# Performance work log

Measured on AMD Instinct MI355X. Metric: run time of the kernel, lower is better.

Reference implementation:

```python
import jax, jax.numpy as jnp
import numpy as np

MIN_NORM = 1e-15
PROJ_EPS = 4e-3   # HGCN PoincareBall eps for float32
C = 1.0
N_NODES = 100000
DEG = 5
F_IN = 128


def _artanh(x):
    return jnp.arctanh(jnp.clip(x, -1.0 + 1e-7, 1.0 - 1e-7))


def _norm(x):
    # clamped L2 norm over last dim, keepdims
    return jnp.maximum(jnp.sqrt(jnp.sum(x * x, axis=-1, keepdims=True)), MIN_NORM)


def proj(x, c):
    norm = _norm(x)
    maxnorm = (1.0 - PROJ_EPS) / jnp.sqrt(c)
    return jnp.where(norm > maxnorm, x / norm * maxnorm, x)


def expmap0(u, c):
    sc = jnp.sqrt(c)
    un = _norm(u)
    return jnp.tanh(sc * un) * u / (sc * un)


def logmap0(p, c):
    sc = jnp.sqrt(c)
    pn = _norm(p)
    return p / pn / sc * _artanh(sc * pn)


def mobius_matvec(m, x, c):
    # HGCN convention: mx = x @ m^T
    sc = jnp.sqrt(c)
    x_norm = _norm(x)
    mx = x @ m.T
    mx_norm = _norm(mx)
    res = jnp.tanh(mx_norm / x_norm * _artanh(sc * x_norm)) * mx / (mx_norm * sc)
    zero = jnp.all(mx == 0, axis=-1, keepdims=True)
    return jnp.where(zero, jnp.zeros_like(res), res)


def setup_inputs() -> dict:
    key = jax.random.key(0)
    k1, k2, k3, k4 = jax.random.split(key, 4)
    x = jax.random.normal(k1, (N_NODES, F_IN), jnp.float32) * 0.1
    gain = 1.414
    W = jax.random.normal(k2, (F_IN, F_IN), jnp.float32) * gain * np.sqrt(2.0 / (F_IN + F_IN))
    a = jax.random.normal(k3, (1, 2 * F_IN), jnp.float32) * gain * np.sqrt(2.0 / (1 + 2 * F_IN))
    # edge list: every node has DEG out-edges so row-sum normalization is safe
    src = jnp.repeat(jnp.arange(N_NODES, dtype=jnp.int32), DEG)
    dst = jax.random.randint(k4, (N_NODES * DEG,), 0, N_NODES, jnp.int32)
    edge = jnp.stack([src, dst])  # [2, E]
    return {"x": x, "edge": edge, "W": W, "a": a}


def reference(x, edge, W, a):
    c = C
    N = x.shape[0]
    # h = logmap0(proj(mobius_matvec(x, W)))  -> [F, N] (module's transposed layout)
    h = logmap0(proj(mobius_matvec(x, W, c), c), c)
    src, dst = edge[0], edge[1]
    # per-edge gather: [2F, E]
    edge_h = jnp.concatenate([h[:, src], h[:, dst]], axis=0)
    edge_h = proj(expmap0(edge_h, c), c)
    # mobius_matvec(edge_h.T, a) -> a @ edge_h : [1, E] -> [E]
    ee = jnp.squeeze(mobius_matvec(edge_h.T, a, c))
    ee = logmap0(proj(ee, c), c)
    ee = jnp.exp(-jax.nn.gelu(ee, approximate=False))  # positive edge weights
    # sparse spmm row-sum and aggregation (scatter-add by source node)
    e_rowsum = jax.ops.segment_sum(ee, src, num_segments=N)                     # [N]
    h_prime = jax.ops.segment_sum(ee[:, None] * h.T[dst], src, num_segments=N)  # [N, F]
    h_prime = h_prime / e_rowsum[:, None]
    return proj(expmap0(jax.nn.elu(h_prime), c), c)
```

## Files before the change

### kernel.cpp

```cpp
#include <hip/hip_runtime.h>
#include <math.h>

#define F 128
#define DEG 5
#define TM 128
#define MAXNORM_D 0.996
#define MIN_NORM_D 1e-15

typedef float f32x4 __attribute__((ext_vector_type(4)));
typedef short s16x8 __attribute__((ext_vector_type(8)));

__device__ inline double atanh_clip(double v) {
    v = fmin(fmax(v, -1.0 + 1e-7), 1.0 - 1e-7);
    return atanh(v);
}

__device__ inline void load_lds16(const void* g, void* l) {
    __builtin_amdgcn_global_load_lds((const __attribute__((address_space(1))) void*)g,
                                     (__attribute__((address_space(3))) void*)l, 16, 0, 0);
}

__device__ inline void split2(float v0, float v1, unsigned& hi, unsigned& lo) {
    unsigned b0 = __float_as_uint(v0), b1 = __float_as_uint(v1);
    unsigned h0 = (b0 + 0x8000u) >> 16;
    unsigned h1 = (b1 + 0x8000u) >> 16;
    float l0 = v0 - __uint_as_float(h0 << 16);
    float l1 = v1 - __uint_as_float(h1 << 16);
    hi = h0 | (h1 << 16);
    lo = (__float_as_uint(l0) >> 16) | (__float_as_uint(l1) & 0xFFFF0000u);
}

__global__ __launch_bounds__(256) void k_ph(const float* __restrict__ W,
                                            uint4* __restrict__ Wfh, uint4* __restrict__ Wfl,
                                            const int* __restrict__ edge, int* __restrict__ cnt, int E) {
    if (blockIdx.x < 8) {
        int tid = blockIdx.x * 256 + threadIdx.x;
        int c = tid >> 9;
        int tp = (tid >> 6) & 7;
        int lane = tid & 63;
        int f = tp * 16 + (lane & 15);
        int k = c * 32 + (lane >> 4) * 8;
        const float* wp = W + f * F + k;
        unsigned h[4], l[4];
#pragma unroll
        for (int p = 0; p < 4; p++) split2(wp[2 * p], wp[2 * p + 1], h[p], l[p]);
        Wfh[tid] = make_uint4(h[0], h[1], h[2], h[3]);
        Wfl[tid] = make_uint4(l[0], l[1], l[2], l[3]);
    } else {
        int e = (blockIdx.x - 8) * 256 + threadIdx.x;
        if (e < E) atomicAdd(&cnt[edge[E + e]], 1);
    }
}

__global__ __launch_bounds__(512, 4) void k_gemm(const float* __restrict__ x,
                                                 const uint4* __restrict__ Wfh, const uint4* __restrict__ Wfl,
                                                 const int* __restrict__ cnt, float* __restrict__ y,
                                                 float* __restrict__ ssum2, float* __restrict__ wsum2, int N) {
    __shared__ uint4 Wh_s[2048];
    __shared__ uint4 Wl_s[2048];
    __shared__ float red_ss[F];
    __shared__ float red_ws[F];
    __shared__ int cntL[TM];

    int t = threadIdx.x;
    int lane = t & 63;
    int w = t >> 6;
    int n0 = blockIdx.x * TM;

    if (t < F) { red_ss[t] = 0.f; red_ws[t] = 0.f; }
    if (t < TM) { int n = n0 + t; cntL[t] = (n < N) ? cnt[n] : 0; }

#pragma unroll
    for (int r = 0; r < 4; r++) {
        int off = (r * 512 + t) * 16;
        load_lds16((const char*)Wfh + off, (char*)Wh_s + off);
    }
#pragma unroll
    for (int r = 0; r < 4; r++) {
        int off = (r * 512 + t) * 16;
        load_lds16((const char*)Wfl + off, (char*)Wl_s + off);
    }

    int row = n0 + w * 16 + (lane & 15);
    if (row > N - 1) row = N - 1;
    const float* xr = x + (size_t)row * F + (lane >> 4) * 8;

    float4 av0[4], av1[4];
#pragma unroll
    for (int c = 0; c < 4; c++) {
        av0[c] = *(const float4*)(xr + c * 32);
        av1[c] = *(const float4*)(xr + c * 32 + 4);
    }

    f32x4 acc[8];
#pragma unroll
    for (int i = 0; i < 8; i++) acc[i] = (f32x4){0.f, 0.f, 0.f, 0.f};

    __syncthreads();

#pragma unroll
    for (int c = 0; c < 4; c++) {
        unsigned h[4], l[4];
        split2(av0[c].x, av0[c].y, h[0], l[0]);
        split2(av0[c].z, av0[c].w, h[1], l[1]);
        split2(av1[c].x, av1[c].y, h[2], l[2]);
        split2(av1[c].z, av1[c].w, h[3], l[3]);
        s16x8 a_hi = __builtin_bit_cast(s16x8, make_uint4(h[0], h[1], h[2], h[3]));
        s16x8 a_lo = __builtin_bit_cast(s16x8, make_uint4(l[0], l[1], l[2], l[3]));
#pragma unroll
        for (int tp = 0; tp < 8; tp++) {
            s16x8 bh = __builtin_bit_cast(s16x8, Wh_s[(c * 8 + tp) * 64 + lane]);
            s16x8 bl = __builtin_bit_cast(s16x8, Wl_s[(c * 8 + tp) * 64 + lane]);
            acc[tp] = __builtin_amdgcn_mfma_f32_16x16x32_bf16(a_hi, bh, acc[tp], 0, 0, 0);
            acc[tp] = __builtin_amdgcn_mfma_f32_16x16x32_bf16(a_lo, bh, acc[tp], 0, 0, 0);
            acc[tp] = __builtin_amdgcn_mfma_f32_16x16x32_bf16(a_hi, bl, acc[tp], 0, 0, 0);
        }
    }

    int fb = lane & 15;
    int rg = lane >> 4;
#pragma unroll
    for (int tp = 0; tp < 8; tp++) {
        int f = tp * 16 + fb;
        float sv = 0.f, wv = 0.f;
#pragma unroll
        for (int r = 0; r < 4; r++) {
            int lr = w * 16 + rg * 4 + r;
            int n = n0 + lr;
            float v = acc[tp][r];
            if (n < N) {
                y[(size_t)n * F + f] = v;
                sv += v * v;
                wv += (float)cntL[lr] * v * v;
            }
        }
        sv += __shfl_xor(sv, 16, 64); sv += __shfl_xor(sv, 32, 64);
        wv += __shfl_xor(wv, 16, 64); wv += __shfl_xor(wv, 32, 64);
        if (lane < 16) {
            atomicAdd(&red_ss[f], sv);
            atomicAdd(&red_ws[f], wv);
        }
    }
    __syncthreads();
    if (t < F) {
        atomicAdd(&ssum2[t], red_ss[t]);
        atomicAdd(&wsum2[t], red_ws[t]);
    }
}

__global__ __launch_bounds__(256) void k_scalars(const float* __restrict__ W, const float* __restrict__ a,
                                                 const float* __restrict__ ssum2, const float* __restrict__ wsum2,
                                                 float* __restrict__ s_arr, float* __restrict__ asrc,
                                                 float* __restrict__ adst, double* __restrict__ an_out) {
    int t = threadIdx.x;
    double av = (double)a[t];
    av *= av;
#pragma unroll
    for (int off = 32; off; off >>= 1) av += __shfl_down(av, off, 64);
    __shared__ double wred[4];
    if ((t & 63) == 0) wred[t >> 6] = av;
    __syncthreads();
    double an = fmax(sqrt(wred[0] + wred[1] + wred[2] + wred[3]), MIN_NORM_D);
    if (t == 0) an_out[0] = an;

    if (t < F) {
        double wn2 = 0.0;
        for (int k = 0; k < F; k++) { double w = (double)W[t * F + k]; wn2 += w * w; }
        double wn = fmax(sqrt(wn2), MIN_NORM_D);
        double mxnf = fmax(sqrt((double)ssum2[t]), MIN_NORM_D);
        double tt = tanh(mxnf / wn * atanh_clip(wn));
        double rn = fmax(tt, MIN_NORM_D);
        double pf = (rn > MAXNORM_D) ? MAXNORM_D / rn : 1.0;
        double pn = rn * pf;
        double s = (tt / mxnf) * pf * atanh_clip(pn) / pn;
        s_arr[t] = (float)s;

        double un_s = fmax(s * sqrt((double)DEG * (double)ssum2[t]), MIN_NORM_D);
        double th_s = tanh(un_s);
        double rn2 = fmax(th_s, MIN_NORM_D);
        double pf2 = (rn2 > MAXNORM_D) ? MAXNORM_D / rn2 : 1.0;
        double q_s = s * (th_s / un_s) * pf2;
        asrc[t] = (float)((double)a[t] * q_s);

        double un_d = fmax(s * sqrt((double)wsum2[t]), MIN_NORM_D);
        double th_d = tanh(un_d);
        double rn3 = fmax(th_d, MIN_NORM_D);
        double pf3 = (rn3 > MAXNORM_D) ? MAXNORM_D / rn3 : 1.0;
        double q_d = s * (th_d / un_d) * pf3;
        adst[t] = (float)((double)a[F + t] * q_d);
    }
}

__global__ __launch_bounds__(256) void k_pq(const float* __restrict__ y, const float* __restrict__ asrc,
                                            const float* __restrict__ adst, float* __restrict__ P,
                                            float* __restrict__ Q, int N) {
    __shared__ float as4[F], ad4[F];
    int t = threadIdx.x;
    if (t < F) { as4[t] = asrc[t]; ad4[t] = adst[t]; }
    __syncthreads();
    int lane = t & 31;
    int n = blockIdx.x * 8 + (t >> 5);
    if (n < N) {
        float4 yv = *(const float4*)&y[(size_t)n * F + lane * 4];
        float4 av = *(const float4*)&as4[lane * 4];
        float4 bv = *(const float4*)&ad4[lane * 4];
        float p = yv.x * av.x + yv.y * av.y + yv.z * av.z + yv.w * av.w;
        float q = yv.x * bv.x + yv.y * bv.y + yv.z * bv.z + yv.w * bv.w;
#pragma unroll
        for (int off = 16; off; off >>= 1) {
            p += __shfl_down(p, off, 32);
            q += __shfl_down(q, off, 32);
        }
        if (lane == 0) { P[n] = p; Q[n] = q; }
    }
}

__global__ __launch_bounds__(256) void k_edge(const int* __restrict__ edge, const float* __restrict__ P,
                                              const float* __restrict__ Q, float* __restrict__ ee_pre,
                                              double* __restrict__ mxn2, int E) {
    int t = threadIdx.x;
    int e = blockIdx.x * 256 + t;
    double local = 0.0;
    if (e < E) {
        int s = e / DEG;
        int d = edge[E + e];
        float v = P[s] + Q[d];
        ee_pre[e] = v;
        local = (double)v * (double)v;
    }
#pragma unroll
    for (int off = 32; off; off >>= 1) local += __shfl_down(local, off, 64);
    __shared__ double wsum[4];
    if ((t & 63) == 0) wsum[t >> 6] = local;
    __syncthreads();
    if (t == 0) atomicAdd(mxn2, wsum[0] + wsum[1] + wsum[2] + wsum[3]);
}

__global__ __launch_bounds__(256) void k_wagg(const int* __restrict__ edge, const float* __restrict__ y,
                                              const float* __restrict__ ee_pre,
                                              const double* __restrict__ an_p, const double* __restrict__ mxn2_p,
                                              const float* __restrict__ s_arr,
                                              float* __restrict__ out, int N, int E) {
    __shared__ float wsh[8 * DEG];
    __shared__ int dsh[8 * DEG];
    __shared__ float gS;
    int t = threadIdx.x;
    int n_base = blockIdx.x * 8;

    if (t == 0) {
        double an = an_p[0];
        double mxn = fmax(sqrt(mxn2_p[0]), MIN_NORM_D);
        double t2 = tanh(mxn / an * atanh_clip(an));
        double f2 = t2 / mxn;
        double rnp = fmax(t2, MIN_NORM_D);
        double pfp = (rnp > MAXNORM_D) ? MAXNORM_D / rnp : 1.0;
        double pnp = rnp * pfp;
        gS = (float)(f2 * pfp * atanh_clip(pnp) / pnp);
    }
    __syncthreads();

    if (t < 8 * DEG) {
        int n = n_base + t / DEG;
        float w = 0.f; int d = 0;
        if (n < N) {
            int e = n * DEG + (t % DEG);
            float xg = gS * ee_pre[e];
            float gl = 0.5f * xg * (1.f + erff(xg * 0.70710678f));
            w = expf(-gl);
            d = edge[E + e];
        }
        wsh[t] = w;
        dsh[t] = d << 7;
    }
    __syncthreads();

    int grp = t >> 5;
    int lane = t & 31;
    int n = n_base + grp;
    if (n >= N) return;

    float rowsum = wsh[grp * DEG + 0] + wsh[grp * DEG + 1] + wsh[grp * DEG + 2]
                 + wsh[grp * DEG + 3] + wsh[grp * DEG + 4];
    float inv = 1.f / rowsum;

    int fo = lane * 4;
    float4 acc = make_float4(0.f, 0.f, 0.f, 0.f);
#pragma unroll
    for (int j = 0; j < DEG; j++) {
        float w = wsh[grp * DEG + j];
        int d = dsh[grp * DEG + j];
        float4 yv = *(const float4*)&y[d + fo];
        acc.x = fmaf(w, yv.x, acc.x);
        acc.y = fmaf(w, yv.y, acc.y);
        acc.z = fmaf(w, yv.z, acc.z);
        acc.w = fmaf(w, yv.w, acc.w);
    }
    float4 s4 = *(const float4*)&s_arr[fo];
    float4 el;
    float hx = s4.x * acc.x * inv; el.x = (hx > 0.f) ? hx : expm1f(hx);
    float hy = s4.y * acc.y * inv; el.y = (hy > 0.f) ? hy : expm1f(hy);
    float hz = s4.z * acc.z * inv; el.z = (hz > 0.f) ? hz : expm1f(hz);
    float hw = s4.w * acc.w * inv; el.w = (hw > 0.f) ? hw : expm1f(hw);

    float ss = el.x * el.x + el.y * el.y + el.z * el.z + el.w * el.w;
#pragma unroll
    for (int off = 16; off; off >>= 1) ss += __shfl_xor(ss, off, 32);

    float un = fmaxf(sqrtf(ss), 1e-15f);
    float th = tanhf(un);
    float sc = th / un;
    float rn = fmaxf(th, 1e-15f);
    if (rn > 0.996f) sc *= 0.996f / rn;
    float4 o = make_float4(el.x * sc, el.y * sc, el.z * sc, el.w * sc);
    *(float4*)&out[(size_t)n * F + fo] = o;
}

extern "C" void kernel_launch(void* const* d_in, const int* in_sizes, int n_in,
                              void* d_out, int out_size, void* d_ws, size_t ws_size,
                              hipStream_t stream) {
    const float* x = (const float*)d_in[0];
    const int* edge = (const int*)d_in[1];
    const float* W = (const float*)d_in[2];
    const float* a = (const float*)d_in[3];
    float* out = (float*)d_out;
    int N = in_sizes[0] / F;
    int E = in_sizes[1] / 2;

    char* ws = (char*)d_ws;
    size_t off = 0;
    float* y = (float*)(ws + off);       off += (size_t)N * F * 4;
    uint4* Wfh = (uint4*)(ws + off);     off += 2048 * 16;
    uint4* Wfl = (uint4*)(ws + off);     off += 2048 * 16;
    float* ee_pre = (float*)(ws + off);  off += (size_t)E * 4;
    float* P = (float*)(ws + off);       off += (size_t)N * 4;
    float* Q = (float*)(ws + off);       off += (size_t)N * 4;
    char* zbase = ws + off;
    int* cnt = (int*)(ws + off);         off += (size_t)N * 4;
    float* ssum2 = (float*)(ws + off);   off += 512;
    float* wsum2 = (float*)(ws + off);   off += 512;
    double* mxn2 = (double*)(ws + off);  off += 8;
    size_t zlen = (size_t)((ws + off) - zbase);
    double* an_p = (double*)(ws + off);  off += 8;
    float* s_arr = (float*)(ws + off);   off += 512;
    float* asrc = (float*)(ws + off);    off += 512;
    float* adst = (float*)(ws + off);    off += 512;

    hipMemsetAsync(zbase, 0, zlen, stream);
    k_ph<<<8 + (E + 255) / 256, 256, 0, stream>>>(W, Wfh, Wfl, edge, cnt, E);
    k_gemm<<<(N + TM - 1) / TM, 512, 0, stream>>>(x, Wfh, Wfl, cnt, y, ssum2, wsum2, N);
    k_scalars<<<1, 256, 0, stream>>>(W, a, ssum2, wsum2, s_arr, asrc, adst, an_p);
    k_pq<<<(N + 7) / 8, 256, 0, stream>>>(y, asrc, adst, P, Q, N);
    k_edge<<<(E + 255) / 256, 256, 0, stream>>>(edge, P, Q, ee_pre, mxn2, E);
    k_wagg<<<(N + 7) / 8, 256, 0, stream>>>(edge, y, ee_pre, an_p, mxn2, s_arr, out, N, E);
}
```

Measured before the change: 240.9 us.

## Use grid-stride loops, bank gemm column reductions, and shuffle-based weighted aggregation

Converts the count, P/Q, edge and aggregation kernels to fixed-size grid-stride launches so fewer blocks are scheduled. The gemm's per-column sum atomics are spread over 8 banks by block index, which cuts contention, and k_scalars sums the banks. k_wagg now uses 8 lanes per node with shuffles in place of shared memory and a block barrier, and each lane handles 16 features. The k_edge atomic count drops, at the cost of longer per-thread loops and less latency hiding per node.

```diff
diff --git a/kernel.cpp b/kernel.cpp
--- a/kernel.cpp
+++ b/kernel.cpp
@@ -47,8 +47,9 @@
         Wfh[tid] = make_uint4(h[0], h[1], h[2], h[3]);
         Wfl[tid] = make_uint4(l[0], l[1], l[2], l[3]);
     } else {
-        int e = (blockIdx.x - 8) * 256 + threadIdx.x;
-        if (e < E) atomicAdd(&cnt[edge[E + e]], 1);
+        int stride = (gridDim.x - 8) * 256;
+        for (int e = (blockIdx.x - 8) * 256 + threadIdx.x; e < E; e += stride)
+            atomicAdd(&cnt[edge[E + e]], 1);
     }
 }
 
@@ -143,8 +144,9 @@
     }
     __syncthreads();
     if (t < F) {
-        atomicAdd(&ssum2[t], red_ss[t]);
-        atomicAdd(&wsum2[t], red_ws[t]);
+        int bank = (blockIdx.x & 7) * F;
+        atomicAdd(&ssum2[bank + t], red_ss[t]);
+        atomicAdd(&wsum2[bank + t], red_ws[t]);
     }
 }
 
@@ -164,10 +166,14 @@
     if (t == 0) an_out[0] = an;
 
     if (t < F) {
+        float ss2f = 0.f, ws2f = 0.f;
+#pragma unroll
+        for (int b = 0; b < 8; b++) { ss2f += ssum2[b * F + t]; ws2f += wsum2[b * F + t]; }
+
         double wn2 = 0.0;
         for (int k = 0; k < F; k++) { double w = (double)W[t * F + k]; wn2 += w * w; }
         double wn = fmax(sqrt(wn2), MIN_NORM_D);
-        double mxnf = fmax(sqrt((double)ssum2[t]), MIN_NORM_D);
+        double mxnf = fmax(sqrt((double)ss2f), MIN_NORM_D);
         double tt = tanh(mxnf / wn * atanh_clip(wn));
         double rn = fmax(tt, MIN_NORM_D);
         double pf = (rn > MAXNORM_D) ? MAXNORM_D / rn : 1.0;
@@ -175,14 +181,14 @@
         double s = (tt / mxnf) * pf * atanh_clip(pn) / pn;
         s_arr[t] = (float)s;
 
-        double un_s = fmax(s * sqrt((double)DEG * (double)ssum2[t]), MIN_NORM_D);
+        double un_s = fmax(s * sqrt((double)DEG * (double)ss2f), MIN_NORM_D);
         double th_s = tanh(un_s);
         double rn2 = fmax(th_s, MIN_NORM_D);
         double pf2 = (rn2 > MAXNORM_D) ? MAXNORM_D / rn2 : 1.0;
         double q_s = s * (th_s / un_s) * pf2;
         asrc[t] = (float)((double)a[t] * q_s);
 
-        double un_d = fmax(s * sqrt((double)wsum2[t]), MIN_NORM_D);
+        double un_d = fmax(s * sqrt((double)ws2f), MIN_NORM_D);
         double th_d = tanh(un_d);
         double rn3 = fmax(th_d, MIN_NORM_D);
         double pf3 = (rn3 > MAXNORM_D) ? MAXNORM_D / rn3 : 1.0;
@@ -199,19 +205,21 @@
     if (t < F) { as4[t] = asrc[t]; ad4[t] = adst[t]; }
     __syncthreads();
     int lane = t & 31;
-    int n = blockIdx.x * 8 + (t >> 5);
-    if (n < N) {
-        float4 yv = *(const float4*)&y[(size_t)n * F + lane * 4];
-        float4 av = *(const float4*)&as4[lane * 4];
-        float4 bv = *(const float4*)&ad4[lane * 4];
-        float p = yv.x * av.x + yv.y * av.y + yv.z * av.z + yv.w * av.w;
-        float q = yv.x * bv.x + yv.y * bv.y + yv.z * bv.z + yv.w * bv.w;
-#pragma unroll
-        for (int off = 16; off; off >>= 1) {
-            p += __shfl_down(p, off, 32);
-            q += __shfl_down(q, off, 32);
-        }
-        if (lane == 0) { P[n] = p; Q[n] = q; }
+    float4 av = *(const float4*)&as4[lane * 4];
+    float4 bv = *(const float4*)&ad4[lane * 4];
+    for (int nb = blockIdx.x * 8; nb < N; nb += gridDim.x * 8) {
+        int n = nb + (t >> 5);
+        if (n < N) {
+            float4 yv = *(const float4*)&y[(size_t)n * F + lane * 4];
+            float p = yv.x * av.x + yv.y * av.y + yv.z * av.z + yv.w * av.w;
+            float q = yv.x * bv.x + yv.y * bv.y + yv.z * bv.z + yv.w * bv.w;
+#pragma unroll
+            for (int off = 16; off; off >>= 1) {
+                p += __shfl_down(p, off, 32);
+                q += __shfl_down(q, off, 32);
+            }
+            if (lane == 0) { P[n] = p; Q[n] = q; }
+        }
     }
 }
 
@@ -219,14 +227,16 @@
                                               const float* __restrict__ Q, float* __restrict__ ee_pre,
                                               double* __restrict__ mxn2, int E) {
     int t = threadIdx.x;
-    int e = blockIdx.x * 256 + t;
     double local = 0.0;
-    if (e < E) {
-        int s = e / DEG;
-        int d = edge[E + e];
-        float v = P[s] + Q[d];
-        ee_pre[e] = v;
-        local = (double)v * (double)v;
+    for (int e0 = blockIdx.x * 256; e0 < E; e0 += gridDim.x * 256) {
+        int e = e0 + t;
+        if (e < E) {
+            int s = e / DEG;
+            int d = edge[E + e];
+            float v = P[s] + Q[d];
+            ee_pre[e] = v;
+            local += (double)v * (double)v;
+        }
     }
 #pragma unroll
     for (int off = 32; off; off >>= 1) local += __shfl_down(local, off, 64);
@@ -241,12 +251,8 @@
                                               const double* __restrict__ an_p, const double* __restrict__ mxn2_p,
                                               const float* __restrict__ s_arr,
                                               float* __restrict__ out, int N, int E) {
-    __shared__ float wsh[8 * DEG];
-    __shared__ int dsh[8 * DEG];
     __shared__ float gS;
     int t = threadIdx.x;
-    int n_base = blockIdx.x * 8;
-
     if (t == 0) {
         double an = an_p[0];
         double mxn = fmax(sqrt(mxn2_p[0]), MIN_NORM_D);
@@ -258,61 +264,85 @@
         gS = (float)(f2 * pfp * atanh_clip(pnp) / pnp);
     }
     __syncthreads();
-
-    if (t < 8 * DEG) {
-        int n = n_base + t / DEG;
+    float g = gS;
+
+    int lane = t & 63;
+    int sub = lane & 7;
+    int slot = t >> 3;
+    int gbase = lane & ~7;
+
+    float4 s4[4];
+#pragma unroll
+    for (int p = 0; p < 4; p++) s4[p] = *(const float4*)&s_arr[p * 32 + sub * 4];
+
+    for (int nb = blockIdx.x * 32; nb < N; nb += gridDim.x * 32) {
+        int n = nb + slot;
+        bool active = (n < N);
+        int nc = active ? n : N - 1;
+
         float w = 0.f; int d = 0;
-        if (n < N) {
-            int e = n * DEG + (t % DEG);
-            float xg = gS * ee_pre[e];
+        if (sub < DEG) {
+            int e = nc * DEG + sub;
+            float xg = g * ee_pre[e];
             float gl = 0.5f * xg * (1.f + erff(xg * 0.70710678f));
             w = expf(-gl);
-            d = edge[E + e];
-        }
-        wsh[t] = w;
-        dsh[t] = d << 7;
-    }
-    __syncthreads();
-
-    int grp = t >> 5;
-    int lane = t & 31;
-    int n = n_base + grp;
-    if (n >= N) return;
-
-    float rowsum = wsh[grp * DEG + 0] + wsh[grp * DEG + 1] + wsh[grp * DEG + 2]
-                 + wsh[grp * DEG + 3] + wsh[grp * DEG + 4];
-    float inv = 1.f / rowsum;
-
-    int fo = lane * 4;
-    float4 acc = make_float4(0.f, 0.f, 0.f, 0.f);
-#pragma unroll
-    for (int j = 0; j < DEG; j++) {
-        float w = wsh[grp * DEG + j];
-        int d = dsh[grp * DEG + j];
-        float4 yv = *(const float4*)&y[d + fo];
-        acc.x = fmaf(w, yv.x, acc.x);
-        acc.y = fmaf(w, yv.y, acc.y);
-        acc.z = fmaf(w, yv.z, acc.z);
-        acc.w = fmaf(w, yv.w, acc.w);
-    }
-    float4 s4 = *(const float4*)&s_arr[fo];
-    float4 el;
-    float hx = s4.x * acc.x * inv; el.x = (hx > 0.f) ? hx : expm1f(hx);
-    float hy = s4.y * acc.y * inv; el.y = (hy > 0.f) ? hy : expm1f(hy);
-    float hz = s4.z * acc.z * inv; el.z = (hz > 0.f) ? hz : expm1f(hz);
-    float hw = s4.w * acc.w * inv; el.w = (hw > 0.f) ? hw : expm1f(hw);
-
-    float ss = el.x * el.x + el.y * el.y + el.z * el.z + el.w * el.w;
-#pragma unroll
-    for (int off = 16; off; off >>= 1) ss += __shfl_xor(ss, off, 32);
-
-    float un = fmaxf(sqrtf(ss), 1e-15f);
-    float th = tanhf(un);
-    float sc = th / un;
-    float rn = fmaxf(th, 1e-15f);
-    if (rn > 0.996f) sc *= 0.996f / rn;
-    float4 o = make_float4(el.x * sc, el.y * sc, el.z * sc, el.w * sc);
-    *(float4*)&out[(size_t)n * F + fo] = o;
+            d = edge[E + e] << 7;
+        }
+        float wj[DEG]; int dj[DEG];
+#pragma unroll
+        for (int j = 0; j < DEG; j++) {
+            wj[j] = __shfl(w, gbase + j, 64);
+            dj[j] = __shfl(d, gbase + j, 64);
+        }
+        float rowsum = wj[0] + wj[1] + wj[2] + wj[3] + wj[4];
+        float inv = 1.f / rowsum;
+
+        float4 acc[4];
+#pragma unroll
+        for (int p = 0; p < 4; p++) acc[p] = make_float4(0.f, 0.f, 0.f, 0.f);
+#pragma unroll
+        for (int j = 0; j < DEG; j++) {
+            const float* yp = y + dj[j] + sub * 4;
+            float wv = wj[j];
+#pragma unroll
+            for (int p = 0; p < 4; p++) {
+                float4 yv = *(const float4*)(yp + p * 32);
+                acc[p].x = fmaf(wv, yv.x, acc[p].x);
+                acc[p].y = fmaf(wv, yv.y, acc[p].y);
+                acc[p].z = fmaf(wv, yv.z, acc[p].z);
+                acc[p].w = fmaf(wv, yv.w, acc[p].w);
+            }
+        }
+
+        float4 el[4];
+        float ss = 0.f;
+#pragma unroll
+        for (int p = 0; p < 4; p++) {
+            float h;
+            h = s4[p].x * acc[p].x * inv; el[p].x = (h > 0.f) ? h : expm1f(h);
+            h = s4[p].y * acc[p].y * inv; el[p].y = (h > 0.f) ? h : expm1f(h);
+            h = s4[p].z * acc[p].z * inv; el[p].z = (h > 0.f) ? h : expm1f(h);
+            h = s4[p].w * acc[p].w * inv; el[p].w = (h > 0.f) ? h : expm1f(h);
+            ss += el[p].x * el[p].x + el[p].y * el[p].y + el[p].z * el[p].z + el[p].w * el[p].w;
+        }
+        ss += __shfl_xor(ss, 1, 64);
+        ss += __shfl_xor(ss, 2, 64);
+        ss += __shfl_xor(ss, 4, 64);
+
+        float un = fmaxf(sqrtf(ss), 1e-15f);
+        float th = tanhf(un);
+        float sc = th / un;
+        float rn = fmaxf(th, 1e-15f);
+        if (rn > 0.996f) sc *= 0.996f / rn;
+        if (active) {
+            float* op = out + (size_t)n * F + sub * 4;
+#pragma unroll
+            for (int p = 0; p < 4; p++) {
+                float4 o = make_float4(el[p].x * sc, el[p].y * sc, el[p].z * sc, el[p].w * sc);
+                *(float4*)(op + p * 32) = o;
+            }
+        }
+    }
 }
 
 extern "C" void kernel_launch(void* const* d_in, const int* in_sizes, int n_in,
@@ -336,8 +366,8 @@
     float* Q = (float*)(ws + off);       off += (size_t)N * 4;
     char* zbase = ws + off;
     int* cnt = (int*)(ws + off);         off += (size_t)N * 4;
-    float* ssum2 = (float*)(ws + off);   off += 512;
-    float* wsum2 = (float*)(ws + off);   off += 512;
+    float* ssum2 = (float*)(ws + off);   off += 8 * F * 4;
+    float* wsum2 = (float*)(ws + off);   off += 8 * F * 4;
     double* mxn2 = (double*)(ws + off);  off += 8;
     size_t zlen = (size_t)((ws + off) - zbase);
     double* an_p = (double*)(ws + off);  off += 8;
@@ -346,10 +376,10 @@
     float* adst = (float*)(ws + off);    off += 512;
 
     hipMemsetAsync(zbase, 0, zlen, stream);
-    k_ph<<<8 + (E + 255) / 256, 256, 0, stream>>>(W, Wfh, Wfl, edge, cnt, E);
+    k_ph<<<8 + 1024, 256, 0, stream>>>(W, Wfh, Wfl, edge, cnt, E);
     k_gemm<<<(N + TM - 1) / TM, 512, 0, stream>>>(x, Wfh, Wfl, cnt, y, ssum2, wsum2, N);
     k_scalars<<<1, 256, 0, stream>>>(W, a, ssum2, wsum2, s_arr, asrc, adst, an_p);
-    k_pq<<<(N + 7) / 8, 256, 0, stream>>>(y, asrc, adst, P, Q, N);
-    k_edge<<<(E + 255) / 256, 256, 0, stream>>>(edge, P, Q, ee_pre, mxn2, E);
-    k_wagg<<<(N + 7) / 8, 256, 0, stream>>>(edge, y, ee_pre, an_p, mxn2, s_arr, out, N, E);
-}
+    k_pq<<<2048, 256, 0, stream>>>(y, asrc, adst, P, Q, N);
+    k_edge<<<1024, 256, 0, stream>>>(edge, P, Q, ee_pre, mxn2, E);
+    k_wagg<<<2048, 256, 0, stream>>>(edge, y, ee_pre, an_p, mxn2, s_arr, out, N, E);
+}
```

New measurement: 222.6 us. -7.6%, faster.
